# Optimization experiments

Measured on AMD Instinct MI355X. Metric: run time of the kernel, lower is better.

The kernel has to match this reference:

```python
import jax, jax.numpy as jnp
import numpy as np

MAX_DIST = 50.0
NO_NEIGHBORS = 0.0
# feature order: [dx, dy, size_a, size_b, angle]; angle mark is cyclic
FEATURES_RANGE = np.array([50.0, 50.0, 32.0, 32.0, np.pi], dtype=np.float32)
FEATURES_CYCLIC = np.array([False, False, False, False, True])


def setup_inputs() -> dict:
    key = jax.random.key(0)
    ks = jax.random.split(key, 8)
    B, N, M, F, H = 8, 1024, 1024, 5, 4
    points = jax.random.normal(ks[0], (B, N, F), jnp.float32)
    context_points = jax.random.normal(ks[1], (B, M, F), jnp.float32)
    points_mask = jnp.ones((B, N), dtype=bool)
    context_points_mask = jnp.ones((B, M), dtype=bool)
    distance_matrix = jax.random.uniform(ks[2], (B, N, M), jnp.float32) * 100.0
    interactions_mask = jax.random.randint(ks[3], (B, N, M), 0, 2).astype(bool)
    # q_fun MLP: Linear(5,4) -> ReLU -> Linear(4,1) -> Sigmoid
    W1 = jax.random.normal(ks[4], (F, H), jnp.float32) / np.sqrt(F)
    b1 = jnp.zeros((H,), jnp.float32)
    W2 = jax.random.normal(ks[5], (H, 1), jnp.float32) / np.sqrt(H)
    b2 = jnp.zeros((1,), jnp.float32)
    # attention weight model: Linear(5,1)
    Wa = jax.random.normal(ks[6], (F, 1), jnp.float32) / np.sqrt(F)
    ba = jnp.zeros((1,), jnp.float32)
    return dict(points=points, points_mask=points_mask,
                context_points=context_points, context_points_mask=context_points_mask,
                distance_matrix=distance_matrix, interactions_mask=interactions_mask,
                global_max_dist=100,
                W1=W1, b1=b1, W2=W2, b2=b2, Wa=Wa, ba=ba)


def reference(points, points_mask, context_points, context_points_mask,
              distance_matrix, interactions_mask, global_max_dist,
              W1, b1, W2, b2, Wa, ba):
    fr = jnp.asarray(FEATURES_RANGE)
    cyc = jnp.asarray(FEATURES_CYCLIC)
    # pairwise abs feature differences: [B, N, M, 5]
    fd = jnp.abs(points[:, :, None, :] - context_points[:, None, :, :])
    fn = fd / fr
    fc = jnp.remainder(fn, 1.0)
    fc = jnp.minimum(fc, 1.0 - fc)           # cyclic wrap-around distance
    fn = jnp.where(cyc, fc, fn)
    # q_fun MLP + sigmoid -> per-pair similarity energy [B, N, M]
    h = jax.nn.relu(jnp.einsum('bnmf,fh->bnmh', fn, W1) + b1)
    energy = jax.nn.sigmoid(jnp.einsum('bnmh,ho->bnmo', h, W2) + b2)[..., 0]
    # interaction mask, tightened by max_dist when max_dist < global_max_dist
    ib = interactions_mask
    if MAX_DIST < global_max_dist:
        ib = ib & (distance_matrix <= MAX_DIST)
    # masked attention reduce over context axis (dim 2)
    scores = (jnp.einsum('bnmf,fo->bnmo', fn, Wa) + ba)[..., 0]
    scores = jnp.where(ib, scores, -jnp.inf)
    weights = jax.nn.softmax(scores, axis=2)  # all-masked rows -> NaN
    reduced = jnp.sum(weights * energy, axis=2)
    reduced = jnp.nan_to_num(reduced, nan=NO_NEIGHBORS,
                             posinf=NO_NEIGHBORS, neginf=NO_NEIGHBORS)
    return reduced
```

## Files before the change

### kernel.cpp

```cpp
#include <hip/hip_runtime.h>
#include <math.h>

#define BATCH   8
#define NPTS    1024
#define MCTX    1024
#define BN      (BATCH * NPTS)

#define INV_R0  0.02f
#define INV_R1  0.02f
#define INV_R2  0.03125f
#define INV_R3  0.03125f
#define INV_R4  0.3183098861837907f
#define MAX_DIST 50.0f
#define LOG2E   1.4426950408889634f

__global__ __launch_bounds__(512) void sim_kernel(
    const float* __restrict__ points,
    const float* __restrict__ ctx,
    const float* __restrict__ dist,
    const unsigned char* __restrict__ imask,
    const int* __restrict__ gmd_p,
    const float* __restrict__ W1p,
    const float* __restrict__ b1p,
    const float* __restrict__ W2p,
    const float* __restrict__ b2p,
    const float* __restrict__ Wap,
    const float* __restrict__ bap,
    float* __restrict__ out)
{
    __shared__ float sctx[MCTX * 5];
    __shared__ unsigned short q[8][MCTX];

    const int wid  = threadIdx.x >> 6;
    const int lane = threadIdx.x & 63;
    const int row  = blockIdx.x * 8 + wid;
    const int b    = row >> 10;

    {
        const float4* __restrict__ src = (const float4*)(ctx + (size_t)b * MCTX * 5);
        float4* dst = (float4*)sctx;
        for (int i = threadIdx.x; i < (MCTX * 5) / 4; i += 512)
            dst[i] = src[i];
    }
    __syncthreads();

    float w1[20];
#pragma unroll
    for (int i = 0; i < 20; ++i) w1[i] = W1p[i];
    float b1v[4];
#pragma unroll
    for (int j = 0; j < 4; ++j) b1v[j] = b1p[j];
    float w2n[4];
#pragma unroll
    for (int j = 0; j < 4; ++j) w2n[j] = W2p[j] * (-LOG2E);
    const float b2n = b2p[0] * (-LOG2E);
    float wan[5];
#pragma unroll
    for (int f = 0; f < 5; ++f) wan[f] = Wap[f] * LOG2E;
    const float ban = bap[0] * LOG2E;

    const float p0 = points[row * 5 + 0];
    const float p1 = points[row * 5 + 1];
    const float p2 = points[row * 5 + 2];
    const float p3 = points[row * 5 + 3];
    const float p4 = points[row * 5 + 4];

    const bool tighten = (MAX_DIST < (float)gmd_p[0]);
    const float4*        __restrict__ d4 = (const float4*)(dist + (size_t)row * MCTX);
    const unsigned int*  __restrict__ m4 = (const unsigned int*)(imask + (size_t)row * MCTX);

    int tot = 0;
#pragma unroll
    for (int j = 0; j < 4; ++j) {
        const float4       dv = d4[lane + 64 * j];
        const unsigned int mv = m4[lane + 64 * j];
        const float dd[4] = { dv.x, dv.y, dv.z, dv.w };
#pragma unroll
        for (int t = 0; t < 4; ++t) {
            bool ok = ((mv >> (8 * t)) & 0xFFu) != 0u;
            if (tighten) ok = ok && (dd[t] <= MAX_DIST);
            unsigned long long bm = __ballot(ok);
            unsigned rank = __builtin_amdgcn_mbcnt_hi(
                                (unsigned)(bm >> 32),
                                __builtin_amdgcn_mbcnt_lo((unsigned)bm, 0u));
            if (ok) {
                const int m = (lane + 64 * j) * 4 + t;
                q[wid][tot + rank] = (unsigned short)(20 * m);
            }
            tot += (int)__popcll(bm);
        }
    }

    float lsum = 0.0f, asum = 0.0f;
    const char* __restrict__ cbase = (const char*)sctx;
#pragma unroll 2
    for (int i = lane; i < tot; i += 64) {
        const int off = (int)q[wid][i];
        const float* __restrict__ c = (const float*)(cbase + off);
        const float c0 = c[0], c1 = c[1], c2 = c[2], c3 = c[3], c4 = c[4];

        float fn0 = fabsf(p0 - c0) * INV_R0;
        float fn1 = fabsf(p1 - c1) * INV_R1;
        float fn2 = fabsf(p2 - c2) * INV_R2;
        float fn3 = fabsf(p3 - c3) * INV_R3;
        float f4  = __builtin_amdgcn_fractf(fabsf(p4 - c4) * INV_R4);
        float fn4 = fminf(f4, 1.0f - f4);

        float h0 = fmaxf(0.0f, b1v[0] + fn0*w1[0]  + fn1*w1[4]  + fn2*w1[8]  + fn3*w1[12] + fn4*w1[16]);
        float h1 = fmaxf(0.0f, b1v[1] + fn0*w1[1]  + fn1*w1[5]  + fn2*w1[9]  + fn3*w1[13] + fn4*w1[17]);
        float h2 = fmaxf(0.0f, b1v[2] + fn0*w1[2]  + fn1*w1[6]  + fn2*w1[10] + fn3*w1[14] + fn4*w1[18]);
        float h3 = fmaxf(0.0f, b1v[3] + fn0*w1[3]  + fn1*w1[7]  + fn2*w1[11] + fn3*w1[15] + fn4*w1[19]);

        float zn = b2n + h0*w2n[0] + h1*w2n[1] + h2*w2n[2] + h3*w2n[3];
        float energy = __builtin_amdgcn_rcpf(1.0f + __builtin_amdgcn_exp2f(zn));

        float sc = ban + fn0*wan[0] + fn1*wan[1] + fn2*wan[2] + fn3*wan[3] + fn4*wan[4];
        float e  = __builtin_amdgcn_exp2f(sc);

        lsum += e;
        asum += e * energy;
    }

#pragma unroll
    for (int off = 1; off < 64; off <<= 1) {
        lsum += __shfl_xor(lsum, off, 64);
        asum += __shfl_xor(asum, off, 64);
    }

    if (lane == 0) {
        out[row] = (lsum > 0.0f) ? (asum / lsum) : 0.0f;
    }
}

extern "C" void kernel_launch(void* const* d_in, const int* in_sizes, int n_in,
                              void* d_out, int out_size, void* d_ws, size_t ws_size,
                              hipStream_t stream) {
    const float*         points = (const float*)d_in[0];
    const float*         ctx    = (const float*)d_in[2];
    const float*         dist   = (const float*)d_in[4];
    const unsigned char* imask  = (const unsigned char*)d_in[5];
    const int*           gmd    = (const int*)d_in[6];
    const float*         W1     = (const float*)d_in[7];
    const float*         b1     = (const float*)d_in[8];
    const float*         W2     = (const float*)d_in[9];
    const float*         b2     = (const float*)d_in[10];
    const float*         Wa     = (const float*)d_in[11];
    const float*         ba     = (const float*)d_in[12];
    float*               out    = (float*)d_out;

    dim3 block(512);
    dim3 grid(BN / 8);
    sim_kernel<<<grid, block, 0, stream>>>(points, ctx, dist, imask, gmd,
                                           W1, b1, W2, b2, Wa, ba, out);
}
```

Measured before the change: 16.25 us.

## Split each row across two wavefronts and merge partial softmax sums in LDS

Each row's context range is now split into two halves, each handled by its own wavefront, with the partial sums combined through shared memory. The grid doubles to BN/4 blocks of 512 threads. All global loads are issued up front and the mask bits are packed before the ballot compaction. The intent is more parallelism per row and better latency hiding, at the cost of loading the context into LDS twice as often overall and an extra block-wide sync.

Result: slower. 17.12 us (+5.4%).

```diff
diff --git a/kernel.cpp b/kernel.cpp
--- a/kernel.cpp
+++ b/kernel.cpp
@@ -5,12 +5,13 @@
 #define NPTS    1024
 #define MCTX    1024
 #define BN      (BATCH * NPTS)
+#define HALF    512
 
 #define INV_R0  0.02f
 #define INV_R1  0.02f
 #define INV_R2  0.03125f
 #define INV_R3  0.03125f
-#define INV_R4  0.3183098861837907f
+#define INV_PI  0.3183098861837907f
 #define MAX_DIST 50.0f
 #define LOG2E   1.4426950408889634f
 
@@ -29,11 +30,14 @@
     float* __restrict__ out)
 {
     __shared__ float sctx[MCTX * 5];
-    __shared__ unsigned short q[8][MCTX];
+    __shared__ unsigned short q[8][HALF];
+    __shared__ float smerge[8][2];
 
     const int wid  = threadIdx.x >> 6;
     const int lane = threadIdx.x & 63;
-    const int row  = blockIdx.x * 8 + wid;
+    const int rloc = wid >> 1;
+    const int half = wid & 1;
+    const int row  = blockIdx.x * 4 + rloc;
     const int b    = row >> 10;
 
     {
@@ -66,29 +70,46 @@
     const float p4 = points[row * 5 + 4];
 
     const bool tighten = (MAX_DIST < (float)gmd_p[0]);
-    const float4*        __restrict__ d4 = (const float4*)(dist + (size_t)row * MCTX);
-    const unsigned int*  __restrict__ m4 = (const unsigned int*)(imask + (size_t)row * MCTX);
+    const int  mbase = half * HALF;
+    const float4*       __restrict__ d4 = (const float4*)(dist  + (size_t)row * MCTX + mbase);
+    const unsigned int* __restrict__ m4 = (const unsigned int*)(imask + (size_t)row * MCTX + mbase);
+
+    float4 dv0 = d4[lane];
+    float4 dv1 = d4[lane + 64];
+    unsigned int mv0 = m4[lane];
+    unsigned int mv1 = m4[lane + 64];
+
+    unsigned okbits = 0;
+    {
+        const float dd0[4] = { dv0.x, dv0.y, dv0.z, dv0.w };
+        const float dd1[4] = { dv1.x, dv1.y, dv1.z, dv1.w };
+#pragma unroll
+        for (int t = 0; t < 4; ++t) {
+            bool ok0 = ((mv0 >> (8 * t)) & 0xFFu) != 0u;
+            bool ok1 = ((mv1 >> (8 * t)) & 0xFFu) != 0u;
+            if (tighten) {
+                ok0 = ok0 && (dd0[t] <= MAX_DIST);
+                ok1 = ok1 && (dd1[t] <= MAX_DIST);
+            }
+            okbits |= ok0 ? (1u << t)       : 0u;
+            okbits |= ok1 ? (1u << (4 + t)) : 0u;
+        }
+    }
 
     int tot = 0;
 #pragma unroll
-    for (int j = 0; j < 4; ++j) {
-        const float4       dv = d4[lane + 64 * j];
-        const unsigned int mv = m4[lane + 64 * j];
-        const float dd[4] = { dv.x, dv.y, dv.z, dv.w };
-#pragma unroll
-        for (int t = 0; t < 4; ++t) {
-            bool ok = ((mv >> (8 * t)) & 0xFFu) != 0u;
-            if (tighten) ok = ok && (dd[t] <= MAX_DIST);
-            unsigned long long bm = __ballot(ok);
-            unsigned rank = __builtin_amdgcn_mbcnt_hi(
-                                (unsigned)(bm >> 32),
-                                __builtin_amdgcn_mbcnt_lo((unsigned)bm, 0u));
-            if (ok) {
-                const int m = (lane + 64 * j) * 4 + t;
-                q[wid][tot + rank] = (unsigned short)(20 * m);
-            }
-            tot += (int)__popcll(bm);
+    for (int k = 0; k < 8; ++k) {
+        const int j = k >> 2, t = k & 3;
+        const bool ok = (okbits >> (j * 4 + t)) & 1u;
+        unsigned long long bm = __ballot(ok);
+        unsigned rank = __builtin_amdgcn_mbcnt_hi(
+                            (unsigned)(bm >> 32),
+                            __builtin_amdgcn_mbcnt_lo((unsigned)bm, 0u));
+        if (ok) {
+            const int m = mbase + (lane + 64 * j) * 4 + t;
+            q[wid][tot + rank] = (unsigned short)(20 * m);
         }
+        tot += (int)__popcll(bm);
     }
 
     float lsum = 0.0f, asum = 0.0f;
@@ -103,8 +124,8 @@
         float fn1 = fabsf(p1 - c1) * INV_R1;
         float fn2 = fabsf(p2 - c2) * INV_R2;
         float fn3 = fabsf(p3 - c3) * INV_R3;
-        float f4  = __builtin_amdgcn_fractf(fabsf(p4 - c4) * INV_R4);
-        float fn4 = fminf(f4, 1.0f - f4);
+        float g   = __builtin_amdgcn_fractf(fabsf(p4 - c4) * INV_PI);
+        float fn4 = fminf(g, 1.0f - g);
 
         float h0 = fmaxf(0.0f, b1v[0] + fn0*w1[0]  + fn1*w1[4]  + fn2*w1[8]  + fn3*w1[12] + fn4*w1[16]);
         float h1 = fmaxf(0.0f, b1v[1] + fn0*w1[1]  + fn1*w1[5]  + fn2*w1[9]  + fn3*w1[13] + fn4*w1[17]);
@@ -118,7 +139,7 @@
         float e  = __builtin_amdgcn_exp2f(sc);
 
         lsum += e;
-        asum += e * energy;
+        asum = fmaf(e, energy, asum);
     }
 
 #pragma unroll
@@ -128,7 +149,14 @@
     }
 
     if (lane == 0) {
-        out[row] = (lsum > 0.0f) ? (asum / lsum) : 0.0f;
+        smerge[wid][0] = lsum;
+        smerge[wid][1] = asum;
+    }
+    __syncthreads();
+    if (half == 0 && lane == 0) {
+        const float L = smerge[wid][0] + smerge[wid + 1][0];
+        const float A = smerge[wid][1] + smerge[wid + 1][1];
+        out[row] = (L > 0.0f) ? (A / L) : 0.0f;
     }
 }
 
@@ -149,7 +177,7 @@
     float*               out    = (float*)d_out;
 
     dim3 block(512);
-    dim3 grid(BN / 8);
+    dim3 grid(BN / 4);
     sim_kernel<<<grid, block, 0, stream>>>(points, ctx, dist, imask, gmd,
                                            W1, b1, W2, b2, Wa, ba, out);
 }
```

## Restructure context staging as float4+scalar SoA and fold feature scales into weights

Applied to the files above, without the earlier changes.

Context points are repacked in shared memory into a float4 array plus a separate pre-scaled angle array, so the inner loop uses one 16-byte LDS load and one scalar load per context point. Per-feature range reciprocals are folded into the MLP and attention weights, and the angle is pre-divided by pi, removing multiplies from the inner loop. The distance and mask global loads are issued before the barrier so they overlap the shared-memory staging, and the mask test is computed into a bitmask before the ballot compaction. Weight folding slightly changes floating-point rounding, and the context staging now uses strided scalar global loads instead of float4 copies.

Result: faster. 15.47 us (-4.8%).

```diff
diff --git a/kernel.cpp b/kernel.cpp
--- a/kernel.cpp
+++ b/kernel.cpp
@@ -10,7 +10,7 @@
 #define INV_R1  0.02f
 #define INV_R2  0.03125f
 #define INV_R3  0.03125f
-#define INV_R4  0.3183098861837907f
+#define INV_PI  0.3183098861837907f
 #define MAX_DIST 50.0f
 #define LOG2E   1.4426950408889634f
 
@@ -28,7 +28,8 @@
     const float* __restrict__ bap,
     float* __restrict__ out)
 {
-    __shared__ float sctx[MCTX * 5];
+    __shared__ float4         sA[MCTX];
+    __shared__ float          s4[MCTX];
     __shared__ unsigned short q[8][MCTX];
 
     const int wid  = threadIdx.x >> 6;
@@ -36,17 +37,34 @@
     const int row  = blockIdx.x * 8 + wid;
     const int b    = row >> 10;
 
-    {
-        const float4* __restrict__ src = (const float4*)(ctx + (size_t)b * MCTX * 5);
-        float4* dst = (float4*)sctx;
-        for (int i = threadIdx.x; i < (MCTX * 5) / 4; i += 512)
-            dst[i] = src[i];
-    }
+    const float* __restrict__ cb = ctx + (size_t)b * MCTX * 5;
+    const int m0 = threadIdx.x, m1 = threadIdx.x + 512;
+    const float r00 = cb[m0*5+0], r01 = cb[m0*5+1], r02 = cb[m0*5+2],
+                r03 = cb[m0*5+3], r04 = cb[m0*5+4];
+    const float r10 = cb[m1*5+0], r11 = cb[m1*5+1], r12 = cb[m1*5+2],
+                r13 = cb[m1*5+3], r14 = cb[m1*5+4];
+
+    const float4*       __restrict__ d4  = (const float4*)(dist + (size_t)row * MCTX);
+    const unsigned int* __restrict__ m4p = (const unsigned int*)(imask + (size_t)row * MCTX);
+    float4 dv0 = d4[lane],       dv1 = d4[lane + 64],
+           dv2 = d4[lane + 128], dv3 = d4[lane + 192];
+    unsigned int mv0 = m4p[lane],       mv1 = m4p[lane + 64],
+                 mv2 = m4p[lane + 128], mv3 = m4p[lane + 192];
+
+    sA[m0] = make_float4(r00, r01, r02, r03);
+    s4[m0] = r04 * INV_PI;
+    sA[m1] = make_float4(r10, r11, r12, r13);
+    s4[m1] = r14 * INV_PI;
     __syncthreads();
 
-    float w1[20];
+    const float ir[4] = { INV_R0, INV_R1, INV_R2, INV_R3 };
+    float w1s[20];
 #pragma unroll
-    for (int i = 0; i < 20; ++i) w1[i] = W1p[i];
+    for (int f = 0; f < 5; ++f) {
+        const float s = (f < 4) ? ir[f] : 1.0f;
+#pragma unroll
+        for (int j = 0; j < 4; ++j) w1s[f*4+j] = W1p[f*4+j] * s;
+    }
     float b1v[4];
 #pragma unroll
     for (int j = 0; j < 4; ++j) b1v[j] = b1p[j];
@@ -56,69 +74,72 @@
     const float b2n = b2p[0] * (-LOG2E);
     float wan[5];
 #pragma unroll
-    for (int f = 0; f < 5; ++f) wan[f] = Wap[f] * LOG2E;
+    for (int f = 0; f < 5; ++f) wan[f] = Wap[f] * LOG2E * ((f < 4) ? ir[f] : 1.0f);
     const float ban = bap[0] * LOG2E;
 
-    const float p0 = points[row * 5 + 0];
-    const float p1 = points[row * 5 + 1];
-    const float p2 = points[row * 5 + 2];
-    const float p3 = points[row * 5 + 3];
-    const float p4 = points[row * 5 + 4];
+    const float p0 = points[row*5+0], p1 = points[row*5+1], p2 = points[row*5+2],
+                p3 = points[row*5+3], p4s = points[row*5+4] * INV_PI;
 
     const bool tighten = (MAX_DIST < (float)gmd_p[0]);
-    const float4*        __restrict__ d4 = (const float4*)(dist + (size_t)row * MCTX);
-    const unsigned int*  __restrict__ m4 = (const unsigned int*)(imask + (size_t)row * MCTX);
+
+    unsigned okbits = 0;
+    {
+        const float4 dvv[4] = { dv0, dv1, dv2, dv3 };
+        const unsigned int mvv[4] = { mv0, mv1, mv2, mv3 };
+#pragma unroll
+        for (int j = 0; j < 4; ++j) {
+            const float dd[4] = { dvv[j].x, dvv[j].y, dvv[j].z, dvv[j].w };
+#pragma unroll
+            for (int t = 0; t < 4; ++t) {
+                bool ok = ((mvv[j] >> (8*t)) & 0xFFu) != 0u;
+                if (tighten) ok = ok && (dd[t] <= MAX_DIST);
+                okbits |= ok ? (1u << (4*j + t)) : 0u;
+            }
+        }
+    }
 
     int tot = 0;
 #pragma unroll
-    for (int j = 0; j < 4; ++j) {
-        const float4       dv = d4[lane + 64 * j];
-        const unsigned int mv = m4[lane + 64 * j];
-        const float dd[4] = { dv.x, dv.y, dv.z, dv.w };
-#pragma unroll
-        for (int t = 0; t < 4; ++t) {
-            bool ok = ((mv >> (8 * t)) & 0xFFu) != 0u;
-            if (tighten) ok = ok && (dd[t] <= MAX_DIST);
-            unsigned long long bm = __ballot(ok);
-            unsigned rank = __builtin_amdgcn_mbcnt_hi(
-                                (unsigned)(bm >> 32),
-                                __builtin_amdgcn_mbcnt_lo((unsigned)bm, 0u));
-            if (ok) {
-                const int m = (lane + 64 * j) * 4 + t;
-                q[wid][tot + rank] = (unsigned short)(20 * m);
-            }
-            tot += (int)__popcll(bm);
+    for (int k = 0; k < 16; ++k) {
+        const bool ok = (okbits >> k) & 1u;
+        unsigned long long bm = __ballot(ok);
+        unsigned rank = __builtin_amdgcn_mbcnt_hi(
+                            (unsigned)(bm >> 32),
+                            __builtin_amdgcn_mbcnt_lo((unsigned)bm, 0u));
+        if (ok) {
+            const int m = (lane + 64 * (k >> 2)) * 4 + (k & 3);
+            q[wid][tot + rank] = (unsigned short)m;
         }
+        tot += (int)__popcll(bm);
     }
 
     float lsum = 0.0f, asum = 0.0f;
-    const char* __restrict__ cbase = (const char*)sctx;
 #pragma unroll 2
     for (int i = lane; i < tot; i += 64) {
-        const int off = (int)q[wid][i];
-        const float* __restrict__ c = (const float*)(cbase + off);
-        const float c0 = c[0], c1 = c[1], c2 = c[2], c3 = c[3], c4 = c[4];
+        const int m = (int)q[wid][i];
+        const float4 cA  = sA[m];
+        const float  c4v = s4[m];
 
-        float fn0 = fabsf(p0 - c0) * INV_R0;
-        float fn1 = fabsf(p1 - c1) * INV_R1;
-        float fn2 = fabsf(p2 - c2) * INV_R2;
-        float fn3 = fabsf(p3 - c3) * INV_R3;
-        float f4  = __builtin_amdgcn_fractf(fabsf(p4 - c4) * INV_R4);
-        float fn4 = fminf(f4, 1.0f - f4);
+        const float a0 = fabsf(p0 - cA.x);
+        const float a1 = fabsf(p1 - cA.y);
+        const float a2 = fabsf(p2 - cA.z);
+        const float a3 = fabsf(p3 - cA.w);
+        float g   = __builtin_amdgcn_fractf(fabsf(p4s - c4v));
+        float fn4 = fminf(g, 1.0f - g);
 
-        float h0 = fmaxf(0.0f, b1v[0] + fn0*w1[0]  + fn1*w1[4]  + fn2*w1[8]  + fn3*w1[12] + fn4*w1[16]);
-        float h1 = fmaxf(0.0f, b1v[1] + fn0*w1[1]  + fn1*w1[5]  + fn2*w1[9]  + fn3*w1[13] + fn4*w1[17]);
-        float h2 = fmaxf(0.0f, b1v[2] + fn0*w1[2]  + fn1*w1[6]  + fn2*w1[10] + fn3*w1[14] + fn4*w1[18]);
-        float h3 = fmaxf(0.0f, b1v[3] + fn0*w1[3]  + fn1*w1[7]  + fn2*w1[11] + fn3*w1[15] + fn4*w1[19]);
+        float h0 = fmaxf(0.0f, b1v[0] + a0*w1s[0] + a1*w1s[4] + a2*w1s[8]  + a3*w1s[12] + fn4*w1s[16]);
+        float h1 = fmaxf(0.0f, b1v[1] + a0*w1s[1] + a1*w1s[5] + a2*w1s[9]  + a3*w1s[13] + fn4*w1s[17]);
+        float h2 = fmaxf(0.0f, b1v[2] + a0*w1s[2] + a1*w1s[6] + a2*w1s[10] + a3*w1s[14] + fn4*w1s[18]);
+        float h3 = fmaxf(0.0f, b1v[3] + a0*w1s[3] + a1*w1s[7] + a2*w1s[11] + a3*w1s[15] + fn4*w1s[19]);
 
         float zn = b2n + h0*w2n[0] + h1*w2n[1] + h2*w2n[2] + h3*w2n[3];
         float energy = __builtin_amdgcn_rcpf(1.0f + __builtin_amdgcn_exp2f(zn));
 
-        float sc = ban + fn0*wan[0] + fn1*wan[1] + fn2*wan[2] + fn3*wan[3] + fn4*wan[4];
+        float sc = ban + a0*wan[0] + a1*wan[1] + a2*wan[2] + a3*wan[3] + fn4*wan[4];
         float e  = __builtin_amdgcn_exp2f(sc);
 
         lsum += e;
-        asum += e * energy;
+        asum = fmaf(e, energy, asum);
     }
 
 #pragma unroll
```
